# Kernel tuning notes

Measured on AMD Instinct MI355X. Metric: run time of the kernel, lower is better.

Reference implementation:

```python
import jax, jax.numpy as jnp
import numpy as np
from jax import lax

N_NOTES, N_WORDS, BATCH = 64, 256, 32
WORDS_DIM, VOCAB = 128, 50000
OC, FW = 256, 3          # conv output channels, filter width
H, NCLS = 256, 2         # GRU hidden, target classes


def setup_inputs() -> dict:
    key = jax.random.key(0)
    ks = jax.random.split(key, 18)
    s = 0.05
    nrm = lambda k, shp: (jax.random.normal(k, shp, dtype=jnp.float32) * s)
    return {
        "mini_batch": jax.random.randint(ks[0], (N_NOTES, N_WORDS, BATCH), 0, VOCAB),
        "hidden_state": jnp.zeros((2, BATCH, H), jnp.float32),
        "embed_table": nrm(ks[1], (VOCAB, WORDS_DIM)),
        "conv_w": nrm(ks[2], (OC, 1, FW, WORDS_DIM)),
        "conv_b": nrm(ks[3], (OC,)),
        "w_ih_f": nrm(ks[4], (3 * H, OC)), "w_hh_f": nrm(ks[5], (3 * H, H)),
        "b_ih_f": nrm(ks[6], (3 * H,)),   "b_hh_f": nrm(ks[7], (3 * H,)),
        "w_ih_b": nrm(ks[8], (3 * H, OC)), "w_hh_b": nrm(ks[9], (3 * H, H)),
        "b_ih_b": nrm(ks[10], (3 * H,)),  "b_hh_b": nrm(ks[11], (3 * H,)),
        "W_note": nrm(ks[12], (2 * H, 2 * H)),
        "bias_note": nrm(ks[13], (2 * H,)),
        "proj_note": nrm(ks[14], (2 * H,)),
        "lin_w": nrm(ks[15], (NCLS, 2 * H)),
        "lin_b": nrm(ks[16], (NCLS,)),
    }


def _gru_scan(xs, h0, w_ih, w_hh, b_ih, b_hh, reverse=False):
    # xs: [N, B, in], h0: [B, H]; standard PyTorch GRU cell math.
    def step(h, x):
        gi = x @ w_ih.T + b_ih
        gh = h @ w_hh.T + b_hh
        ir, iz, i_n = jnp.split(gi, 3, axis=-1)
        hr, hz, h_n = jnp.split(gh, 3, axis=-1)
        r = jax.nn.sigmoid(ir + hr)
        z = jax.nn.sigmoid(iz + hz)
        n = jnp.tanh(i_n + r * h_n)
        h_new = (1.0 - z) * n + z * h
        return h_new, h_new
    _, ys = lax.scan(step, h0, xs, reverse=reverse)
    return ys  # [N, B, H]


def reference(mini_batch, hidden_state, embed_table, conv_w, conv_b,
              w_ih_f, w_hh_f, b_ih_f, b_hh_f,
              w_ih_b, w_hh_b, b_ih_b, b_hh_b,
              W_note, bias_note, proj_note, lin_w, lin_b):
    N, Wd, B = mini_batch.shape
    toks = mini_batch.transpose(0, 2, 1)                 # [N, B, Wd]
    emb = embed_table[toks]                              # [N, B, Wd, D] -- big gather
    x = emb.reshape(N * B, 1, Wd, WORDS_DIM)             # NCHW
    y = lax.conv_general_dilated(
        x, conv_w, window_strides=(1, 1),
        padding=((FW - 1, FW - 1), (0, 0)),
        dimension_numbers=("NCHW", "OIHW", "NCHW"))     # [N*B, OC, L, 1]
    y = jnp.tanh(y + conv_b[None, :, None, None])[..., 0]  # [N*B, OC, L]
    feat = y.max(axis=2).reshape(N, B, -1)               # max-pool over words -> [N, B, OC]

    out_f = _gru_scan(feat, hidden_state[0], w_ih_f, w_hh_f, b_ih_f, b_hh_f)
    out_b = _gru_scan(feat, hidden_state[1], w_ih_b, w_hh_b, b_ih_b, b_hh_b, reverse=True)
    out_note = jnp.concatenate([out_f, out_b], axis=-1)  # [N, B, 2H]

    # additive attention over notes (fused version of the per-step python loops)
    squish = jnp.tanh(jnp.einsum("nbd,de->nbe", out_note, W_note) + bias_note)
    attn = jnp.einsum("nbe,e->nb", squish, proj_note)    # [N, B]
    note_attn_norm = jax.nn.softmax(attn.T, axis=1)      # [B, N], softmax over notes
    note_attn_vectors = jnp.einsum("nb,nbd->bd", note_attn_norm.T, out_note)  # [B, 2H]
    final_map = note_attn_vectors @ lin_w.T + lin_b      # [B, NCLS]
    return (out_note, note_attn_norm, note_attn_vectors, final_map)
```

## Files before the change

### kernel.cpp

```cpp
#include <hip/hip_runtime.h>

#define NN 64
#define NW 256
#define NB 32
#define WD 128
#define OCH 256
#define HD 256
#define G3 768

typedef __attribute__((ext_vector_type(8))) __bf16 bf16x8;
typedef __attribute__((ext_vector_type(4))) __bf16 bf16x4;
typedef __attribute__((ext_vector_type(4))) float  f32x4;

__device__ __forceinline__ float sigm(float x){ return 1.f/(1.f + __expf(-x)); }
__device__ __forceinline__ float tanh_(float x){
  float xx = fminf(fmaxf(x, -15.f), 15.f);
  float e = __expf(-2.f*xx);
  return (1.f - e)/(1.f + e);
}
__device__ __forceinline__ bf16x8 pack8(f32x4 a, f32x4 b){
  bf16x8 v;
  v[0]=(__bf16)a[0]; v[1]=(__bf16)a[1]; v[2]=(__bf16)a[2]; v[3]=(__bf16)a[3];
  v[4]=(__bf16)b[0]; v[5]=(__bf16)b[1]; v[6]=(__bf16)b[2]; v[7]=(__bf16)b[3];
  return v;
}
__device__ __forceinline__ void gload_lds16(const void* g, void* l){
  __builtin_amdgcn_global_load_lds(
      (const __attribute__((address_space(1))) unsigned int*)g,
      (__attribute__((address_space(3))) unsigned int*)l, 16, 0, 0);
}

#define EMB_ELEMS 6400000
#define CW_ELEMS  98304
__global__ void k0_cvt(const float* __restrict__ emb, const float* __restrict__ cw,
                       __bf16* __restrict__ embb, __bf16* __restrict__ cwb)
{
  long e8 = ((long)blockIdx.x*256 + threadIdx.x)*8;
  if (e8 < EMB_ELEMS) {
    f32x4 a = *(const f32x4*)(emb + e8); f32x4 b = *(const f32x4*)(emb + e8 + 4);
    *(bf16x8*)(embb + e8) = pack8(a, b);
  } else if (e8 < EMB_ELEMS + CW_ELEMS) {
    long o = e8 - EMB_ELEMS;
    f32x4 a = *(const f32x4*)(cw + o); f32x4 b = *(const f32x4*)(cw + o + 4);
    *(bf16x8*)(cwb + o) = pack8(a, b);
  }
}

__global__ __launch_bounds__(512, 2) void k1_conv(
    const int* __restrict__ mb, const __bf16* __restrict__ embb,
    const __bf16* __restrict__ cwb, const float* __restrict__ cb,
    __bf16* __restrict__ feat)
{
  __shared__ int tok[NW];
  __shared__ __bf16 A[274*128];
  const int blk = blockIdx.x, n = blk >> 5, b = blk & 31;
  const int t = threadIdx.x, wv = t >> 6, l = t & 63;
  const int lo = l & 15, hi = l >> 4;
  if (t < NW) tok[t] = mb[(n*NW + t)*NB + b];
  if (t < 288) {
    int rr = t >> 4, c = t & 15;
    int row = (rr < 2) ? rr : (256 + rr);
    f32x4 z = {0.f,0.f,0.f,0.f};
    *(f32x4*)((char*)A + row*256 + c*16) = z;
  }
  __syncthreads();
  #pragma unroll
  for (int rr = 0; rr < 8; ++rr) {
    const int w = wv*32 + rr*4 + hi;
    const int row = w + 2;
    const __bf16* src = embb + (long)tok[w]*WD + ((lo ^ (row & 7)) << 3);
    gload_lds16(src, &A[(wv*32 + rr*4 + 2)*128]);
  }
  __syncthreads();
  const int ocb = wv*32;
  bf16x8 B[2][12];
  #pragma unroll
  for (int nt = 0; nt < 2; ++nt) {
    int oc = ocb + nt*16 + lo;
    #pragma unroll
    for (int kf = 0; kf < 12; ++kf)
      B[nt][kf] = *(const bf16x8*)(cwb + oc*384 + kf*32 + hi*8);
  }
  f32x4 mx0 = {-3e38f,-3e38f,-3e38f,-3e38f}, mx1 = mx0;
  for (int mt = 0; mt < 17; ++mt) {
    bf16x8 Af[12];
    const int lrow = mt*16 + lo;
    #pragma unroll
    for (int kf = 0; kf < 12; ++kf) {
      int prow = lrow + (kf >> 2);
      int ch = (kf & 3)*4 + hi;
      Af[kf] = *(const bf16x8*)((char*)A + prow*256 + ((ch ^ (prow & 7)) << 4));
    }
    f32x4 a0 = {0,0,0,0}, a1 = {0,0,0,0};
    #pragma unroll
    for (int kf = 0; kf < 12; ++kf) {
      a0 = __builtin_amdgcn_mfma_f32_16x16x32_bf16(Af[kf], B[0][kf], a0, 0,0,0);
      a1 = __builtin_amdgcn_mfma_f32_16x16x32_bf16(Af[kf], B[1][kf], a1, 0,0,0);
    }
    const int rbase = mt*16 + hi*4;
    #pragma unroll
    for (int r = 0; r < 4; ++r) {
      if (rbase + r < 258) {
        mx0[r] = fmaxf(mx0[r], a0[r]);
        mx1[r] = fmaxf(mx1[r], a1[r]);
      }
    }
  }
  float v0 = fmaxf(fmaxf(mx0[0], mx0[1]), fmaxf(mx0[2], mx0[3]));
  float v1 = fmaxf(fmaxf(mx1[0], mx1[1]), fmaxf(mx1[2], mx1[3]));
  v0 = fmaxf(v0, __shfl_xor(v0, 16)); v0 = fmaxf(v0, __shfl_xor(v0, 32));
  v1 = fmaxf(v1, __shfl_xor(v1, 16)); v1 = fmaxf(v1, __shfl_xor(v1, 32));
  if (l < 16) {
    const int m = n*NB + b;
    feat[m*OCH + ocb + l]      = (__bf16)tanh_(v0 + cb[ocb + l]);
    feat[m*OCH + ocb + 16 + l] = (__bf16)tanh_(v1 + cb[ocb + 16 + l]);
  }
}

__global__ __launch_bounds__(256, 2) void k2_gi(
    const __bf16* __restrict__ feat,
    const float* __restrict__ wihf, const float* __restrict__ bihf, const float* __restrict__ bhhf,
    const float* __restrict__ wihb, const float* __restrict__ bihb, const float* __restrict__ bhhb,
    float* __restrict__ gi_t)
{
  const int bid = blockIdx.x;
  const int mblk = bid & 31, cblk = bid >> 5;
  const int dir = (cblk >= 12) ? 1 : 0;
  const int jb = (cblk - dir*12)*64;
  const float* wih = dir ? wihb : wihf;
  const float* bih = dir ? bihb : bihf;
  const float* bhh = dir ? bhhb : bhhf;
  const int t = threadIdx.x, wv = t >> 6, l = t & 63;
  const int lo = l & 15, hi = l >> 4;
  const int mbase = mblk*64 + wv*16;
  bf16x8 Af[8];
  #pragma unroll
  for (int kf = 0; kf < 8; ++kf)
    Af[kf] = *(const bf16x8*)(feat + (mbase + lo)*HD + kf*32 + hi*8);
  bf16x8 Bf[4][8];
  #pragma unroll
  for (int nt = 0; nt < 4; ++nt) {
    int j = jb + nt*16 + lo;
    #pragma unroll
    for (int kf = 0; kf < 8; ++kf) {
      const float* src = wih + j*HD + kf*32 + hi*8;
      Bf[nt][kf] = pack8(*(const f32x4*)src, *(const f32x4*)(src + 4));
    }
  }
  f32x4 acc[4];
  #pragma unroll
  for (int nt = 0; nt < 4; ++nt) { f32x4 z = {0,0,0,0}; acc[nt] = z; }
  #pragma unroll
  for (int kf = 0; kf < 8; ++kf)
    #pragma unroll
    for (int nt = 0; nt < 4; ++nt)
      acc[nt] = __builtin_amdgcn_mfma_f32_16x16x32_bf16(Af[kf], Bf[nt][kf], acc[nt], 0,0,0);
  #pragma unroll
  for (int nt = 0; nt < 4; ++nt) {
    int j = jb + nt*16 + lo;
    float bias = bih[j] + (j < 512 ? bhh[j] : 0.f);
    #pragma unroll
    for (int r = 0; r < 4; ++r) {
      int m = mbase + hi*4 + r;
      int note = m >> 5, bb = m & 31;
      gi_t[((((long)dir*NN + note)*2 + (bb >> 4))*G3 + j)*16 + (bb & 15)] = acc[nt][r] + bias;
    }
  }
}

__global__ __launch_bounds__(512, 2) void k3_gru(
    const float* __restrict__ gi_t,
    const float* __restrict__ whhf, const float* __restrict__ bhhf,
    const float* __restrict__ whhb, const float* __restrict__ bhhb,
    const float* __restrict__ hid,
    float* __restrict__ out)
{
  const int blk = blockIdx.x;
  const int dir = blk >> 1, mtb = blk & 1;
  const float* whh = dir ? whhb : whhf;
  const float* bhh = dir ? bhhb : bhhf;
  const int t = threadIdx.x, wv = t >> 6, l = t & 63;
  const int lo = l & 15, hi = l >> 4;
  __shared__ __bf16 hb[2][16*256];
  __shared__ float  gib[2][G3*16];

  bf16x8 Bf[3][2][8];
  #pragma unroll
  for (int g = 0; g < 3; ++g)
    #pragma unroll
    for (int q = 0; q < 2; ++q) {
      const int col = g*256 + wv*32 + q*16 + lo;
      #pragma unroll
      for (int kf = 0; kf < 8; ++kf) {
        const float* src = whh + col*HD + kf*32 + hi*8;
        Bf[g][q][kf] = pack8(*(const f32x4*)src, *(const f32x4*)(src + 4));
      }
    }
  const float bnh0 = bhh[512 + wv*32 + lo];
  const float bnh1 = bhh[512 + wv*32 + 16 + lo];

  f32x4 h[2];
  #pragma unroll
  for (int q = 0; q < 2; ++q)
    #pragma unroll
    for (int r = 0; r < 4; ++r)
      h[q][r] = hid[dir*(NB*HD) + (mtb*16 + hi*4 + r)*HD + wv*32 + q*16 + lo];

  #pragma unroll
  for (int q = 0; q < 2; ++q) {
    const int j = wv*32 + q*16 + lo;
    #pragma unroll
    for (int r = 0; r < 4; ++r) {
      const int row = hi*4 + r;
      *(__bf16*)((char*)&hb[0][0] + row*512 + (((j >> 3) ^ (row & 7)) << 4) + (j & 7)*2)
          = (__bf16)h[q][r];
    }
  }

  const long gtile = ((long)(dir*NN + (dir ? 63 : 0))*2 + mtb)*(G3*16);
  #pragma unroll
  for (int p = 0; p < 6; ++p) {
    const int c = (p*8 + wv)*256;
    gload_lds16(gi_t + gtile + c + l*4, &gib[0][c]);
  }
  __syncthreads();

  int cur = 0;
  for (int st = 0; st < 64; ++st) {
    const int note = dir ? 63 - st : st;
    if (st < 63) {
      const int nnote = dir ? 62 - st : st + 1;
      const long gt2 = ((long)(dir*NN + nnote)*2 + mtb)*(G3*16);
      #pragma unroll
      for (int p = 0; p < 6; ++p) {
        const int c = (p*8 + wv)*256;
        gload_lds16(gi_t + gt2 + c + l*4, &gib[cur ^ 1][c]);
      }
    }
    f32x4 acc[3][2];
    #pragma unroll
    for (int g = 0; g < 3; ++g)
      #pragma unroll
      for (int q = 0; q < 2; ++q) { f32x4 z = {0,0,0,0}; acc[g][q] = z; }
    const char* hbc = (const char*)&hb[cur][0];
    #pragma unroll
    for (int kf = 0; kf < 8; ++kf) {
      const int ch = kf*4 + hi;
      bf16x8 Afr = *(const bf16x8*)(hbc + lo*512 + ((ch ^ (lo & 7)) << 4));
      #pragma unroll
      for (int g = 0; g < 3; ++g)
        #pragma unroll
        for (int q = 0; q < 2; ++q)
          acc[g][q] = __builtin_amdgcn_mfma_f32_16x16x32_bf16(Afr, Bf[g][q][kf], acc[g][q], 0,0,0);
    }
    char* hbn = (char*)&hb[cur ^ 1][0];
    const float* gcur = &gib[cur][0];
    #pragma unroll
    for (int q = 0; q < 2; ++q) {
      const int jH = wv*32 + q*16 + lo;
      f32x4 ir  = *(const f32x4*)(gcur + (jH        )*16 + hi*4);
      f32x4 iz  = *(const f32x4*)(gcur + (jH + 256  )*16 + hi*4);
      f32x4 in_ = *(const f32x4*)(gcur + (jH + 512  )*16 + hi*4);
      const float bn = q ? bnh1 : bnh0;
      #pragma unroll
      for (int r = 0; r < 4; ++r) {
        float rr = sigm(ir[r] + acc[0][q][r]);
        float zz = sigm(iz[r] + acc[1][q][r]);
        float nn = tanh_(in_[r] + rr*(acc[2][q][r] + bn));
        float hv = (1.f - zz)*nn + zz*h[q][r];
        h[q][r] = hv;
        const int row = hi*4 + r;
        *(__bf16*)(hbn + row*512 + (((jH >> 3) ^ (row & 7)) << 4) + (jH & 7)*2) = (__bf16)hv;
        out[(long)(note*NB + mtb*16 + row)*512 + dir*HD + jH] = hv;
      }
    }
    asm volatile("s_waitcnt vmcnt(8) lgkmcnt(0)\n\ts_barrier" ::: "memory");
    cur ^= 1;
  }
}

__global__ void k4pre(const float* __restrict__ Wn, __bf16* __restrict__ Wt){
  int idx = blockIdx.x*256 + threadIdx.x;
  int e = idx >> 9, d = idx & 511;
  Wt[e*512 + d] = (__bf16)Wn[d*512 + e];
}

__global__ __launch_bounds__(256, 2) void k4a(
    const float* __restrict__ onf, const __bf16* __restrict__ Wt,
    const float* __restrict__ bn, const float* __restrict__ pj,
    float* __restrict__ attn)
{
  const int mbase = blockIdx.x*16;
  const int t = threadIdx.x, wv = t >> 6, l = t & 63;
  bf16x8 Af[16];
  #pragma unroll
  for (int kf = 0; kf < 16; ++kf) {
    const float* src = onf + (mbase + (l & 15))*512 + kf*32 + (l >> 4)*8;
    Af[kf] = pack8(*(const f32x4*)src, *(const f32x4*)(src + 4));
  }
  float aa0=0, aa1=0, aa2=0, aa3=0;
  #pragma unroll 1
  for (int ntl = 0; ntl < 8; ++ntl) {
    const int e = wv*128 + ntl*16 + (l & 15);
    const float be = bn[e], pe = pj[e];
    f32x4 acc = {0,0,0,0};
    #pragma unroll
    for (int kf = 0; kf < 16; ++kf) {
      bf16x8 Bfr = *(const bf16x8*)(Wt + e*512 + kf*32 + (l >> 4)*8);
      acc = __builtin_amdgcn_mfma_f32_16x16x32_bf16(Af[kf], Bfr, acc, 0,0,0);
    }
    aa0 += tanh_(acc[0] + be)*pe;
    aa1 += tanh_(acc[1] + be)*pe;
    aa2 += tanh_(acc[2] + be)*pe;
    aa3 += tanh_(acc[3] + be)*pe;
  }
  #pragma unroll
  for (int msk = 8; msk >= 1; msk >>= 1) {
    aa0 += __shfl_xor(aa0, msk); aa1 += __shfl_xor(aa1, msk);
    aa2 += __shfl_xor(aa2, msk); aa3 += __shfl_xor(aa3, msk);
  }
  __shared__ float part[4][16];
  if ((l & 15) == 0) {
    int rb = (l >> 4)*4;
    part[wv][rb+0]=aa0; part[wv][rb+1]=aa1; part[wv][rb+2]=aa2; part[wv][rb+3]=aa3;
  }
  __syncthreads();
  if (t < 16) attn[mbase + t] = part[0][t] + part[1][t] + part[2][t] + part[3][t];
}

__global__ __launch_bounds__(512) void k4b(
    const float* __restrict__ attn, const float* __restrict__ lw, const float* __restrict__ lb,
    float* __restrict__ out)
{
  const int b = blockIdx.x, t = threadIdx.x;
  __shared__ float wl[64];
  __shared__ float vl[512];
  if (t < 64) {
    float a = attn[t*NB + b];
    float mx = a;
    #pragma unroll
    for (int msk = 32; msk >= 1; msk >>= 1) mx = fmaxf(mx, __shfl_xor(mx, msk));
    float ex = __expf(a - mx);
    float s = ex;
    #pragma unroll
    for (int msk = 32; msk >= 1; msk >>= 1) s += __shfl_xor(s, msk);
    float w = ex / s;
    out[1048576 + b*64 + t] = w;
    wl[t] = w;
  }
  __syncthreads();
  {
    float acc = 0.f;
    #pragma unroll 1
    for (int n = 0; n < 64; ++n) acc += wl[n]*out[(n*NB + b)*512 + t];
    out[1050624 + b*512 + t] = acc;
    vl[t] = acc;
  }
  __syncthreads();
  if (t < 128) {
    int c = t >> 6, ln = t & 63;
    float p = 0.f;
    for (int d = ln; d < 512; d += 64) p += vl[d]*lw[c*512 + d];
    #pragma unroll
    for (int msk = 32; msk >= 1; msk >>= 1) p += __shfl_xor(p, msk);
    if (ln == 0) out[1067008 + b*2 + c] = p + lb[c];
  }
}

extern "C" void kernel_launch(void* const* d_in, const int* in_sizes, int n_in,
                              void* d_out, int out_size, void* d_ws, size_t ws_size,
                              hipStream_t stream) {
  const int*   mb   = (const int*)d_in[0];
  const float* hid  = (const float*)d_in[1];
  const float* emb  = (const float*)d_in[2];
  const float* cw   = (const float*)d_in[3];
  const float* cb   = (const float*)d_in[4];
  const float* wihf = (const float*)d_in[5];
  const float* whhf = (const float*)d_in[6];
  const float* bihf = (const float*)d_in[7];
  const float* bhhf = (const float*)d_in[8];
  const float* wihb = (const float*)d_in[9];
  const float* whhb = (const float*)d_in[10];
  const float* bihb = (const float*)d_in[11];
  const float* bhhb = (const float*)d_in[12];
  const float* Wn   = (const float*)d_in[13];
  const float* bnote= (const float*)d_in[14];
  const float* pj   = (const float*)d_in[15];
  const float* lw   = (const float*)d_in[16];
  const float* lb   = (const float*)d_in[17];
  float* out = (float*)d_out;
  char* ws = (char*)d_ws;
  __bf16* feat = (__bf16*)ws;
  __bf16* embb = (__bf16*)(ws + 1048576);
  float*  gi_t = (float*)(ws + 1048576);
  float*  attn = (float*)(ws + 13848576);
  __bf16* Wt   = (__bf16*)(ws + 13856768);
  __bf16* cwb  = (__bf16*)(ws + 14380800);

  k0_cvt<<<3173, 256, 0, stream>>>(emb, cw, embb, cwb);
  k1_conv<<<2048, 512, 0, stream>>>(mb, embb, cwb, cb, feat);
  k2_gi<<<768, 256, 0, stream>>>(feat, wihf, bihf, bhhf, wihb, bihb, bhhb, gi_t);
  k4pre<<<1024, 256, 0, stream>>>(Wn, Wt);
  k3_gru<<<4, 512, 0, stream>>>(gi_t, whhf, bhhf, whhb, bhhb, hid, out);
  k4a<<<128, 256, 0, stream>>>(out, Wt, bnote, pj, attn);
  k4b<<<32, 512, 0, stream>>>(attn, lw, lb, out);
}
```

Measured before the change: 615.8 us.

## Store GRU input gates in bf16 and split recurrence across 16 waves

The precomputed input-gate tensor is now written in bf16 instead of fp32, which halves its global traffic and LDS footprint. The serial GRU kernel moves from 8 to 16 waves per block, so each wave owns 16 hidden columns instead of 32. That halves the MFMA chain and the gate math per wave on every one of the 64 sequential steps. The cost is lower precision on the input gates and a barrier across twice as many waves at each step.

Measured after the change: 606.9 us. About the same (-1.4%).

```diff
diff --git a/kernel.cpp b/kernel.cpp
--- a/kernel.cpp
+++ b/kernel.cpp
@@ -121,7 +121,7 @@
     const __bf16* __restrict__ feat,
     const float* __restrict__ wihf, const float* __restrict__ bihf, const float* __restrict__ bhhf,
     const float* __restrict__ wihb, const float* __restrict__ bihb, const float* __restrict__ bhhb,
-    float* __restrict__ gi_t)
+    __bf16* __restrict__ gi_t)
 {
   const int bid = blockIdx.x;
   const int mblk = bid & 31, cblk = bid >> 5;
@@ -163,13 +163,14 @@
     for (int r = 0; r < 4; ++r) {
       int m = mbase + hi*4 + r;
       int note = m >> 5, bb = m & 31;
-      gi_t[((((long)dir*NN + note)*2 + (bb >> 4))*G3 + j)*16 + (bb & 15)] = acc[nt][r] + bias;
-    }
-  }
-}
-
-__global__ __launch_bounds__(512, 2) void k3_gru(
-    const float* __restrict__ gi_t,
+      gi_t[((((long)dir*NN + note)*2 + (bb >> 4))*G3 + j)*16 + (bb & 15)]
+          = (__bf16)(acc[nt][r] + bias);
+    }
+  }
+}
+
+__global__ __launch_bounds__(1024) void k3_gru(
+    const __bf16* __restrict__ gi_t,
     const float* __restrict__ whhf, const float* __restrict__ bhhf,
     const float* __restrict__ whhb, const float* __restrict__ bhhb,
     const float* __restrict__ hid,
@@ -182,66 +183,52 @@
   const int t = threadIdx.x, wv = t >> 6, l = t & 63;
   const int lo = l & 15, hi = l >> 4;
   __shared__ __bf16 hb[2][16*256];
-  __shared__ float  gib[2][G3*16];
-
-  bf16x8 Bf[3][2][8];
-  #pragma unroll
-  for (int g = 0; g < 3; ++g)
-    #pragma unroll
-    for (int q = 0; q < 2; ++q) {
-      const int col = g*256 + wv*32 + q*16 + lo;
-      #pragma unroll
-      for (int kf = 0; kf < 8; ++kf) {
-        const float* src = whh + col*HD + kf*32 + hi*8;
-        Bf[g][q][kf] = pack8(*(const f32x4*)src, *(const f32x4*)(src + 4));
-      }
-    }
-  const float bnh0 = bhh[512 + wv*32 + lo];
-  const float bnh1 = bhh[512 + wv*32 + 16 + lo];
-
-  f32x4 h[2];
-  #pragma unroll
-  for (int q = 0; q < 2; ++q)
-    #pragma unroll
-    for (int r = 0; r < 4; ++r)
-      h[q][r] = hid[dir*(NB*HD) + (mtb*16 + hi*4 + r)*HD + wv*32 + q*16 + lo];
-
-  #pragma unroll
-  for (int q = 0; q < 2; ++q) {
-    const int j = wv*32 + q*16 + lo;
-    #pragma unroll
-    for (int r = 0; r < 4; ++r) {
-      const int row = hi*4 + r;
-      *(__bf16*)((char*)&hb[0][0] + row*512 + (((j >> 3) ^ (row & 7)) << 4) + (j & 7)*2)
-          = (__bf16)h[q][r];
-    }
-  }
-
-  const long gtile = ((long)(dir*NN + (dir ? 63 : 0))*2 + mtb)*(G3*16);
-  #pragma unroll
-  for (int p = 0; p < 6; ++p) {
-    const int c = (p*8 + wv)*256;
-    gload_lds16(gi_t + gtile + c + l*4, &gib[0][c]);
-  }
-  __syncthreads();
+  __shared__ __bf16 gib[2][G3*16];
+
+  const int jl = wv*16 + lo;
+  bf16x8 Bf[3][8];
+  #pragma unroll
+  for (int g = 0; g < 3; ++g) {
+    const int col = g*256 + jl;
+    #pragma unroll
+    for (int kf = 0; kf < 8; ++kf) {
+      const float* src = whh + col*HD + kf*32 + hi*8;
+      Bf[g][kf] = pack8(*(const f32x4*)src, *(const f32x4*)(src + 4));
+    }
+  }
+  const float bnh = bhh[512 + jl];
+
+  float h[4];
+  #pragma unroll
+  for (int r = 0; r < 4; ++r)
+    h[r] = hid[dir*(NB*HD) + (mtb*16 + hi*4 + r)*HD + jl];
+  #pragma unroll
+  for (int r = 0; r < 4; ++r) {
+    const int row = hi*4 + r;
+    *(__bf16*)((char*)&hb[0][0] + row*512 + (((jl >> 3) ^ (row & 7)) << 4) + (jl & 7)*2)
+        = (__bf16)h[r];
+  }
+
+  {
+    const int note0 = dir ? 63 : 0;
+    const __bf16* gt = gi_t + ((long)(dir*NN + note0)*2 + mtb)*(G3*16);
+    gload_lds16(gt + wv*512 + l*8, &gib[0][wv*512]);
+    if (wv < 8) gload_lds16(gt + (16 + wv)*512 + l*8, &gib[0][(16 + wv)*512]);
+  }
+  asm volatile("s_waitcnt vmcnt(0) lgkmcnt(0)\n\ts_barrier" ::: "memory");
 
   int cur = 0;
   for (int st = 0; st < 64; ++st) {
     const int note = dir ? 63 - st : st;
     if (st < 63) {
-      const int nnote = dir ? 62 - st : st + 1;
-      const long gt2 = ((long)(dir*NN + nnote)*2 + mtb)*(G3*16);
-      #pragma unroll
-      for (int p = 0; p < 6; ++p) {
-        const int c = (p*8 + wv)*256;
-        gload_lds16(gi_t + gt2 + c + l*4, &gib[cur ^ 1][c]);
-      }
-    }
-    f32x4 acc[3][2];
-    #pragma unroll
-    for (int g = 0; g < 3; ++g)
-      #pragma unroll
-      for (int q = 0; q < 2; ++q) { f32x4 z = {0,0,0,0}; acc[g][q] = z; }
+      const int nn2 = dir ? 62 - st : st + 1;
+      const __bf16* gt = gi_t + ((long)(dir*NN + nn2)*2 + mtb)*(G3*16);
+      gload_lds16(gt + wv*512 + l*8, &gib[cur ^ 1][wv*512]);
+      if (wv < 8) gload_lds16(gt + (16 + wv)*512 + l*8, &gib[cur ^ 1][(16 + wv)*512]);
+    }
+    f32x4 acc[3];
+    #pragma unroll
+    for (int g = 0; g < 3; ++g) { f32x4 z = {0,0,0,0}; acc[g] = z; }
     const char* hbc = (const char*)&hb[cur][0];
     #pragma unroll
     for (int kf = 0; kf < 8; ++kf) {
@@ -249,32 +236,25 @@
       bf16x8 Afr = *(const bf16x8*)(hbc + lo*512 + ((ch ^ (lo & 7)) << 4));
       #pragma unroll
       for (int g = 0; g < 3; ++g)
-        #pragma unroll
-        for (int q = 0; q < 2; ++q)
-          acc[g][q] = __builtin_amdgcn_mfma_f32_16x16x32_bf16(Afr, Bf[g][q][kf], acc[g][q], 0,0,0);
+        acc[g] = __builtin_amdgcn_mfma_f32_16x16x32_bf16(Afr, Bf[g][kf], acc[g], 0,0,0);
     }
     char* hbn = (char*)&hb[cur ^ 1][0];
-    const float* gcur = &gib[cur][0];
-    #pragma unroll
-    for (int q = 0; q < 2; ++q) {
-      const int jH = wv*32 + q*16 + lo;
-      f32x4 ir  = *(const f32x4*)(gcur + (jH        )*16 + hi*4);
-      f32x4 iz  = *(const f32x4*)(gcur + (jH + 256  )*16 + hi*4);
-      f32x4 in_ = *(const f32x4*)(gcur + (jH + 512  )*16 + hi*4);
-      const float bn = q ? bnh1 : bnh0;
-      #pragma unroll
-      for (int r = 0; r < 4; ++r) {
-        float rr = sigm(ir[r] + acc[0][q][r]);
-        float zz = sigm(iz[r] + acc[1][q][r]);
-        float nn = tanh_(in_[r] + rr*(acc[2][q][r] + bn));
-        float hv = (1.f - zz)*nn + zz*h[q][r];
-        h[q][r] = hv;
-        const int row = hi*4 + r;
-        *(__bf16*)(hbn + row*512 + (((jH >> 3) ^ (row & 7)) << 4) + (jH & 7)*2) = (__bf16)hv;
-        out[(long)(note*NB + mtb*16 + row)*512 + dir*HD + jH] = hv;
-      }
-    }
-    asm volatile("s_waitcnt vmcnt(8) lgkmcnt(0)\n\ts_barrier" ::: "memory");
+    const char* gc = (const char*)&gib[cur][0];
+    bf16x4 ur  = *(const bf16x4*)(gc + jl*32 + hi*8);
+    bf16x4 uz  = *(const bf16x4*)(gc + 8192  + jl*32 + hi*8);
+    bf16x4 un  = *(const bf16x4*)(gc + 16384 + jl*32 + hi*8);
+    #pragma unroll
+    for (int r = 0; r < 4; ++r) {
+      float rr = sigm((float)ur[r] + acc[0][r]);
+      float zz = sigm((float)uz[r] + acc[1][r]);
+      float nn = tanh_((float)un[r] + rr*(acc[2][r] + bnh));
+      float hv = (1.f - zz)*nn + zz*h[r];
+      h[r] = hv;
+      const int row = hi*4 + r;
+      *(__bf16*)(hbn + row*512 + (((jl >> 3) ^ (row & 7)) << 4) + (jl & 7)*2) = (__bf16)hv;
+      out[(long)(note*NB + mtb*16 + row)*512 + dir*HD + jl] = hv;
+    }
+    asm volatile("s_waitcnt vmcnt(4) lgkmcnt(0)\n\ts_barrier" ::: "memory");
     cur ^= 1;
   }
 }
@@ -392,7 +372,7 @@
   char* ws = (char*)d_ws;
   __bf16* feat = (__bf16*)ws;
   __bf16* embb = (__bf16*)(ws + 1048576);
-  float*  gi_t = (float*)(ws + 1048576);
+  __bf16* gi_t = (__bf16*)(ws + 1048576);
   float*  attn = (float*)(ws + 13848576);
   __bf16* Wt   = (__bf16*)(ws + 13856768);
   __bf16* cwb  = (__bf16*)(ws + 14380800);
@@ -401,7 +381,7 @@
   k1_conv<<<2048, 512, 0, stream>>>(mb, embb, cwb, cb, feat);
   k2_gi<<<768, 256, 0, stream>>>(feat, wihf, bihf, bhhf, wihb, bihb, bhhb, gi_t);
   k4pre<<<1024, 256, 0, stream>>>(Wn, Wt);
-  k3_gru<<<4, 512, 0, stream>>>(gi_t, whhf, bhhf, whhb, bhhb, hid, out);
+  k3_gru<<<4, 1024, 0, stream>>>(gi_t, whhf, bhhf, whhb, bhhb, hid, out);
   k4a<<<128, 256, 0, stream>>>(out, Wt, bnote, pj, attn);
   k4b<<<32, 512, 0, stream>>>(attn, lw, lb, out);
 }
```
